# Kernel tuning notes

Hardware: AMD Instinct MI355X
Metric: run time of the kernel (lower is better)

Reference implementation:

```python
import jax, jax.numpy as jnp
import numpy as np

BS, IMG, P, GRID, NPATCH = 4, 224, 14, 16, 256
D, HID, NC, NDIST = 384, 2688, 1000, 7
BETA = 0.07
LN_EPS = 1e-6


def setup_inputs() -> dict:
    key = jax.random.key(0)
    ks = jax.random.split(key, 10)
    feat_target = jax.random.normal(ks[0], (BS, NPATCH, D), jnp.float32)
    feat_ref = jax.random.normal(ks[1], (BS, NPATCH, D), jnp.float32)
    labels_ref = jax.random.randint(ks[2], (BS, 1, IMG, IMG), 0, NC, jnp.int32)
    # distractor permutations of the batch (one per distractor sample)
    perms = jnp.argsort(jax.random.uniform(ks[3], (NDIST, BS)), axis=-1).astype(jnp.int32)
    # projector Mlp (fc1 -> GELU -> fc2), xavier-ish scaling
    fc1_w = jax.random.normal(ks[4], (D, HID), jnp.float32) * (1.0 / np.sqrt(D))
    fc1_b = jnp.zeros((HID,), jnp.float32)
    fc2_w = jax.random.normal(ks[5], (HID, D), jnp.float32) * (1.0 / np.sqrt(HID))
    fc2_b = jnp.zeros((D,), jnp.float32)
    ln_w = jnp.ones((D,), jnp.float32)
    ln_b = jnp.zeros((D,), jnp.float32)
    return {"feat_target": feat_target, "feat_ref": feat_ref, "labels_ref": labels_ref,
            "perms": perms, "fc1_w": fc1_w, "fc1_b": fc1_b, "fc2_w": fc2_w,
            "fc2_b": fc2_b, "ln_w": ln_w, "ln_b": ln_b}


def _layer_norm(x, w, b):
    mu = x.mean(-1, keepdims=True)
    var = jnp.mean((x - mu) ** 2, axis=-1, keepdims=True)
    return (x - mu) * jax.lax.rsqrt(var + LN_EPS) * w + b


def _l2norm(x, eps=1e-12):
    n = jnp.sqrt(jnp.sum(x * x, axis=-1, keepdims=True))
    return x / jnp.maximum(n, eps)


def reference(feat_target, feat_ref, labels_ref, perms, fc1_w, fc1_b, fc2_w, fc2_b, ln_w, ln_b):
    bs = feat_target.shape[0]

    def proj_norm(x):
        h = jax.nn.gelu(x @ fc1_w + fc1_b, approximate=False)  # torch nn.GELU (erf)
        return _layer_norm(h @ fc2_w + fc2_b, ln_w, ln_b)

    ft = proj_norm(feat_target)   # (bs, 256, 384)
    fr = proj_norm(feat_ref)      # (bs, 256, 384)

    # patchify ground truth: (bs,1,224,224) -> (bs, 256, 14*14)
    g = labels_ref.reshape(bs, 1, GRID, P, GRID, P).transpose(0, 2, 4, 1, 3, 5)
    g = g.reshape(bs, NPATCH, P * P)
    # per-patch class histogram / (P*P) == one_hot(...).mean(dim=3), without huge one-hot
    seg = (jnp.arange(NPATCH, dtype=jnp.int32)[None, :, None] * NC + g).reshape(bs, -1)
    counts = jax.vmap(lambda s: jax.ops.segment_sum(
        jnp.ones(s.shape, jnp.float32), s, num_segments=NPATCH * NC))(seg)
    label = counts.reshape(bs, NPATCH, NC) / float(P * P)  # (bs, 256, 1000)

    # distractors: block 0 is identity, blocks 1..NDIST are batch permutations
    all_perm = jnp.concatenate([jnp.arange(bs, dtype=perms.dtype)[None], perms], 0)  # (8, bs)
    lab_d = label[all_perm].transpose(1, 0, 2, 3).reshape(bs, -1, NC)   # (bs, 2048, 1000)
    feat_d = fr[all_perm].transpose(1, 0, 2, 3).reshape(bs, -1, D)      # (bs, 2048, 384)

    # cosine-similarity softmax cross attention (soft kNN over labels)
    q = _l2norm(ft)
    k = _l2norm(feat_d)
    attn = jax.nn.softmax(jnp.einsum('bqd,bkd->bqk', q, k) / BETA, axis=-1)
    label_hat = jnp.einsum('bqk,bkc->bqc', attn, lab_d)                 # (bs, 256, 1000)

    label_hat = label_hat.reshape(bs, GRID, GRID, NC).transpose(0, 3, 1, 2)
    # nearest upsample 16x16 -> 224x224 (scale 14 exactly)
    out = jnp.repeat(jnp.repeat(label_hat, P, axis=2), P, axis=3)
    return out
```

## Files before the change

kernel.cpp:

```cpp
#include <hip/hip_runtime.h>

#define BSZ 4
#define NPATCH 256
#define DIM 384
#define HID 2688
#define NCLS 1000
#define KTOT 2048
#define IMGSZ 224
#define PCH 14
#define GRD 16

static constexpr float INV_BETA = 1.0f / 0.07f;
static constexpr float LN_EPS_F = 1e-6f;

typedef unsigned short u16;
typedef unsigned int   u32;
typedef __attribute__((ext_vector_type(8))) __bf16 bf16x8;
typedef __attribute__((ext_vector_type(4))) float  f32x4;

#define WAITVM(n) asm volatile("s_waitcnt vmcnt(" #n ")" ::: "memory")

__device__ __forceinline__ u16 f2bf(float f) {
    u32 u = __float_as_uint(f);
    return (u16)((u + 0x7FFFu + ((u >> 16) & 1u)) >> 16);
}
__device__ __forceinline__ float bf2f(u16 h) {
    return __uint_as_float(((u32)h) << 16);
}
__device__ __forceinline__ f32x4 mfma16(bf16x8 a, bf16x8 b, f32x4 c) {
    return __builtin_amdgcn_mfma_f32_16x16x32_bf16(a, b, c, 0, 0, 0);
}
__device__ __forceinline__ void gll16(const u16* g, u16* l) {
    __builtin_amdgcn_global_load_lds(
        (const __attribute__((address_space(1))) void*)g,
        (__attribute__((address_space(3))) void*)l, 16, 0, 0);
}
__device__ __forceinline__ bf16x8 ld8(const u16* p) {
    return *(const bf16x8*)p;
}
__device__ __forceinline__ int swz(int row, int cseg) {
    return cseg ^ ((row >> 1) & 3);
}

__device__ __forceinline__ void transpose_split_body(
    const float* __restrict__ In, int R, int C, int bx, int by,
    u16* __restrict__ OutHi, u16* __restrict__ OutLo, float (*tile)[33])
{
    int cx = bx * 32, ry = by * 32;
    int tr = threadIdx.x >> 5, tc = threadIdx.x & 31;
    #pragma unroll
    for (int i = 0; i < 4; ++i)
        tile[tr + i * 8][tc] = In[(size_t)(ry + tr + i * 8) * C + cx + tc];
    __syncthreads();
    #pragma unroll
    for (int i = 0; i < 4; ++i) {
        int orow = cx + tr + i * 8;
        int ocol = ry + tc;
        float v = tile[tc][tr + i * 8];
        u16 h = f2bf(v);
        OutHi[(size_t)orow * R + ocol] = h;
        OutLo[(size_t)orow * R + ocol] = f2bf(v - bf2f(h));
    }
}

__global__ __launch_bounds__(256) void prep_kernel(
    const float* __restrict__ Xt, const float* __restrict__ Xr,
    const float* __restrict__ fc1w, const float* __restrict__ fc2w,
    const int* __restrict__ labels,
    u16* __restrict__ Xhi, u16* __restrict__ Xlo,
    u16* __restrict__ W1Th, u16* __restrict__ W1Tl,
    u16* __restrict__ W2Th, u16* __restrict__ W2Tl,
    u16* __restrict__ LabT)
{
    __shared__ float tile[32][33];
    __shared__ int hist16[16][NCLS];
    int blk = blockIdx.x, t = threadIdx.x;
    if (blk < 768) {
        int e = (blk * 256 + t) * 4;
        const float* src = (e < 1024 * DIM) ? (Xt + e) : (Xr + e - 1024 * DIM);
        float4 v = *(const float4*)src;
        float x[4] = {v.x, v.y, v.z, v.w};
        u16 h[4], l[4];
        #pragma unroll
        for (int i = 0; i < 4; ++i) {
            h[i] = f2bf(x[i]);
            l[i] = f2bf(x[i] - bf2f(h[i]));
        }
        *(uint2*)(Xhi + e) = make_uint2((u32)h[0] | ((u32)h[1] << 16), (u32)h[2] | ((u32)h[3] << 16));
        *(uint2*)(Xlo + e) = make_uint2((u32)l[0] | ((u32)l[1] << 16), (u32)l[2] | ((u32)l[3] << 16));
    } else if (blk < 1776) {
        int i = blk - 768;
        transpose_split_body(fc1w, DIM, HID, i % (HID / 32), i / (HID / 32), W1Th, W1Tl, tile);
    } else if (blk < 2784) {
        int i = blk - 1776;
        transpose_split_body(fc2w, HID, DIM, i % (DIM / 32), i / (DIM / 32), W2Th, W2Tl, tile);
    } else {
        int bp = blk - 2784;
        int b = bp >> 4, py = bp & 15;
        for (int u = t; u < 16 * NCLS; u += 256) ((int*)hist16)[u] = 0;
        __syncthreads();
        const int* lrow = labels + (size_t)b * IMGSZ * IMGSZ + py * PCH * IMGSZ;
        for (int i = t; i < PCH * IMGSZ; i += 256) {
            int lab = lrow[i];
            int px = (i % IMGSZ) / PCH;
            atomicAdd(&hist16[px][lab], 1);
        }
        __syncthreads();
        const float inv = 1.0f / (PCH * PCH);
        for (int u = t; u < 16 * NCLS; u += 256) {
            int c = u >> 4, px = u & 15;
            LabT[((size_t)(b << 10) + c) * 256 + py * 16 + px] =
                f2bf(hist16[px][c] * inv);
        }
    }
}

template<int MODE>
__global__ __launch_bounds__(256) void gemm64(
    const u16* __restrict__ Ahi, const u16* __restrict__ Alo,
    const u16* __restrict__ Bhi, const u16* __restrict__ Blo,
    const float* __restrict__ bias, const int* __restrict__ perms,
    u16* __restrict__ OutHi, u16* __restrict__ OutLo, float* __restrict__ OutF)
{
    constexpr int K  = (MODE == 1) ? HID : DIM;
    constexpr int KS = (MODE == 1) ? HID / 4 : K;
    constexpr int NT = KS / 32;
    constexpr int N  = (MODE == 0) ? HID : (MODE == 1 ? DIM : KTOT);

    __shared__ u16 As_h[3][128 * 32];
    __shared__ u16 As_l[3][128 * 32];
    __shared__ u16 Bs_h[3][64 * 32];
    __shared__ u16 Bs_l[3][64 * 32];

    const int tid = threadIdx.x, lane = tid & 63, wid = tid >> 6;
    const int wm = wid >> 1, wn = wid & 1;
    int n0, m0;
    if constexpr (MODE == 0) {
        int s = (blockIdx.x & 7) * 84 + (blockIdx.x >> 3);
        n0 = (s % 42) * 64;
        m0 = (s / 42) * 128;
    } else {
        n0 = blockIdx.x * 64;
        m0 = blockIdx.y * 128;
    }

    const u16 *a_h, *a_l, *b_h, *b_l;
    if constexpr (MODE == 0) {
        a_h = Ahi + (size_t)m0 * K;   a_l = Alo + (size_t)m0 * K;
        b_h = Bhi + (size_t)n0 * K;   b_l = Blo + (size_t)n0 * K;
    } else if constexpr (MODE == 1) {
        const int kbase = blockIdx.z * KS;
        a_h = Ahi + (size_t)m0 * K + kbase;   a_l = Alo + (size_t)m0 * K + kbase;
        b_h = Bhi + (size_t)n0 * K + kbase;   b_l = Blo + (size_t)n0 * K + kbase;
    } else {
        const int b = blockIdx.z;
        const int d = n0 >> 8;
        const int apd = (d == 0) ? b : perms[(d - 1) * BSZ + b];
        a_h = Ahi + (size_t)(b * NPATCH + m0) * K;
        a_l = Alo + (size_t)(b * NPATCH + m0) * K;
        b_h = Bhi + (size_t)(1024 + apd * NPATCH + (n0 & 255)) * K;
        b_l = Blo + (size_t)(1024 + apd * NPATCH + (n0 & 255)) * K;
    }

    auto stage = [&](int buf, int k0) {
        #pragma unroll
        for (int j = 0; j < 2; ++j) {
            int g = j * 256 + tid;
            int row = g >> 2, cs = g & 3;
            int col = swz(row, cs) << 3;
            gll16(a_h + (size_t)row * K + k0 + col, &As_h[buf][g * 8]);
            gll16(a_l + (size_t)row * K + k0 + col, &As_l[buf][g * 8]);
        }
        {
            int row = tid >> 2, cs = tid & 3;
            int col = swz(row, cs) << 3;
            gll16(b_h + (size_t)row * K + k0 + col, &Bs_h[buf][tid * 8]);
            gll16(b_l + (size_t)row * K + k0 + col, &Bs_l[buf][tid * 8]);
        }
    };

    const int l15 = lane & 15, cq = lane >> 4;
    int aoff[4], boff[2];
    #pragma unroll
    for (int i = 0; i < 4; ++i) {
        int ra = wm * 64 + i * 16 + l15;
        aoff[i] = ra * 32 + swz(ra, cq) * 8;
    }
    #pragma unroll
    for (int j = 0; j < 2; ++j) {
        int rb = wn * 32 + j * 16 + l15;
        boff[j] = rb * 32 + swz(rb, cq) * 8;
    }

    f32x4 acc[4][2] = {};

    auto compute = [&](int buf) {
        bf16x8 ah[4], al[4], bh[2], bl[2];
        #pragma unroll
        for (int i = 0; i < 4; ++i) {
            ah[i] = ld8(&As_h[buf][aoff[i]]);
            al[i] = ld8(&As_l[buf][aoff[i]]);
        }
        #pragma unroll
        for (int j = 0; j < 2; ++j) {
            bh[j] = ld8(&Bs_h[buf][boff[j]]);
            bl[j] = ld8(&Bs_l[buf][boff[j]]);
        }
        #pragma unroll
        for (int mi = 0; mi < 4; ++mi)
            #pragma unroll
            for (int ni = 0; ni < 2; ++ni) {
                acc[mi][ni] = mfma16(ah[mi], bh[ni], acc[mi][ni]);
                acc[mi][ni] = mfma16(ah[mi], bl[ni], acc[mi][ni]);
                acc[mi][ni] = mfma16(al[mi], bh[ni], acc[mi][ni]);
            }
    };

    stage(0, 0);
    stage(1, 32);
    int cur = 0;
    for (int t = 0; t < NT - 1; ++t) {
        WAITVM(6);
        __builtin_amdgcn_s_barrier();
        __builtin_amdgcn_sched_barrier(0);
        if (t + 2 < NT) {
            int nb = cur + 2; if (nb >= 3) nb -= 3;
            stage(nb, (t + 2) * 32);
        }
        compute(cur);
        cur = (cur == 2) ? 0 : cur + 1;
    }
    WAITVM(0);
    __builtin_amdgcn_s_barrier();
    __builtin_amdgcn_sched_barrier(0);
    compute(cur);

    #pragma unroll
    for (int mi = 0; mi < 4; ++mi)
        #pragma unroll
        for (int ni = 0; ni < 2; ++ni)
            #pragma unroll
            for (int r = 0; r < 4; ++r) {
                int gm = m0 + wm * 64 + mi * 16 + cq * 4 + r;
                int gn = n0 + wn * 32 + ni * 16 + l15;
                float v = acc[mi][ni][r];
                if constexpr (MODE == 0) {
                    v += bias[gn];
                    v = 0.5f * v * (1.0f + erff(v * 0.7071067811865476f));
                    u16 h = f2bf(v);
                    OutHi[(size_t)gm * N + gn] = h;
                    OutLo[(size_t)gm * N + gn] = f2bf(v - bf2f(h));
                } else if constexpr (MODE == 1) {
                    OutF[(size_t)blockIdx.z * (2048 * DIM) + (size_t)gm * N + gn] = v;
                } else {
                    float e = expf((v - 1.0f) * INV_BETA);
                    OutHi[((size_t)blockIdx.z * NPATCH + gm) * KTOT + gn] = f2bf(e);
                }
            }
}

__global__ __launch_bounds__(512) void pv_pipe(
    const u16* __restrict__ E, const u16* __restrict__ LabT,
    const int* __restrict__ perms, const float* __restrict__ R,
    float* __restrict__ Lhat)
{
    constexpr int NT = KTOT / 32;
    __shared__ u16 As[3][64 * 32];
    __shared__ u16 Bs[3][64 * 32];
    __shared__ int ap[8];

    const int tid = threadIdx.x, lane = tid & 63, wid = tid >> 6;
    const int wm = wid >> 2, wn = wid & 3;
    const int n0 = blockIdx.x * 64, m0 = blockIdx.y * 64, b = blockIdx.z;
    if (tid < 8) ap[tid] = (tid == 0) ? b : perms[(tid - 1) * BSZ + b];
    __syncthreads();

    const u16* abase = E + (size_t)(b * NPATCH + m0) * KTOT;
    const int cr = (tid & 255) >> 2, ccs = (tid & 255) & 3;
    const int cc = swz(cr, ccs) * 8;

    auto stage = [&](int buf, int k0) {
        if (tid < 256) {
            gll16(abase + (size_t)cr * KTOT + k0 + cc, &As[buf][(tid & 255) * 8]);
        } else {
            int apd = ap[k0 >> 8];
            gll16(LabT + ((size_t)(apd << 10) + n0 + cr) * 256 + (k0 & 255) + cc,
                  &Bs[buf][(tid & 255) * 8]);
        }
    };

    const int l15 = lane & 15, cq = lane >> 4;
    int aoff[2], boff;
    #pragma unroll
    for (int mi = 0; mi < 2; ++mi) {
        int row = wm * 32 + l15 + mi * 16;
        aoff[mi] = row * 32 + swz(row, cq) * 8;
    }
    {
        int row = wn * 16 + l15;
        boff = row * 32 + swz(row, cq) * 8;
    }

    f32x4 acc[2] = {};
    auto compute = [&](int buf) {
        bf16x8 bfr = ld8(&Bs[buf][boff]);
        #pragma unroll
        for (int mi = 0; mi < 2; ++mi) {
            bf16x8 afr = ld8(&As[buf][aoff[mi]]);
            acc[mi] = mfma16(afr, bfr, acc[mi]);
        }
    };

    stage(0, 0);
    stage(1, 32);
    int cur = 0;
    for (int t = 0; t < NT - 1; ++t) {
        WAITVM(1);
        __builtin_amdgcn_s_barrier();
        __builtin_amdgcn_sched_barrier(0);
        if (t + 2 < NT) {
            int nb = cur + 2; if (nb >= 3) nb -= 3;
            stage(nb, (t + 2) * 32);
        }
        compute(cur);
        cur = (cur == 2) ? 0 : cur + 1;
    }
    WAITVM(0);
    __builtin_amdgcn_s_barrier();
    __builtin_amdgcn_sched_barrier(0);
    compute(cur);

    const int gn = n0 + wn * 16 + l15;
    if (gn < NCLS) {
        #pragma unroll
        for (int mi = 0; mi < 2; ++mi)
            #pragma unroll
            for (int r = 0; r < 4; ++r) {
                int gm = m0 + wm * 32 + mi * 16 + ((lane >> 4) << 2) + r;
                float denom = R[(size_t)b * NPATCH + gm];
                Lhat[((size_t)b * NPATCH + gm) * NCLS + gn] = acc[mi][r] / denom;
            }
    }
}

__device__ __forceinline__ float wave_sum(float v) {
    #pragma unroll
    for (int off = 32; off > 0; off >>= 1) v += __shfl_xor(v, off);
    return v;
}

__global__ __launch_bounds__(256) void rowsum_kernel(
    const u16* __restrict__ E, float* __restrict__ R)
{
    int row = blockIdx.x, t = threadIdx.x;
    uint4 u = *(const uint4*)(E + (size_t)row * KTOT + t * 8);
    float s = bf2f(u.x & 0xffff) + bf2f(u.x >> 16)
            + bf2f(u.y & 0xffff) + bf2f(u.y >> 16)
            + bf2f(u.z & 0xffff) + bf2f(u.z >> 16)
            + bf2f(u.w & 0xffff) + bf2f(u.w >> 16);
    s = wave_sum(s);
    __shared__ float red[4];
    if ((t & 63) == 0) red[t >> 6] = s;
    __syncthreads();
    if (t == 0) R[row] = red[0] + red[1] + red[2] + red[3];
}

__global__ __launch_bounds__(256) void ln_l2_kernel(
    const float* __restrict__ P0, const float* __restrict__ fc2b,
    const float* __restrict__ w, const float* __restrict__ b,
    u16* __restrict__ Zhi, u16* __restrict__ Zlo)
{
    const float* P1 = P0 + 1 * 2048 * DIM;
    const float* P2 = P0 + 2 * 2048 * DIM;
    const float* P3 = P0 + 3 * 2048 * DIM;
    int wid = threadIdx.x >> 6, lane = threadIdx.x & 63;
    int row = blockIdx.x * 4 + wid;
    size_t base = (size_t)row * DIM;
    float x[6];
    float s = 0.0f;
    #pragma unroll
    for (int i = 0; i < 6; ++i) {
        int c = lane + 64 * i;
        x[i] = ((P0[base + c] + P1[base + c]) + (P2[base + c] + P3[base + c])) + fc2b[c];
        s += x[i];
    }
    s = wave_sum(s);
    float mu = s * (1.0f / DIM);
    float vs = 0.0f;
    #pragma unroll
    for (int i = 0; i < 6; ++i) { float d = x[i] - mu; vs += d * d; }
    vs = wave_sum(vs);
    float rstd = 1.0f / sqrtf(vs * (1.0f / DIM) + LN_EPS_F);
    float z[6];
    float n2 = 0.0f;
    #pragma unroll
    for (int i = 0; i < 6; ++i) {
        z[i] = (x[i] - mu) * rstd * w[lane + 64 * i] + b[lane + 64 * i];
        n2 += z[i] * z[i];
    }
    n2 = wave_sum(n2);
    float inv = 1.0f / fmaxf(sqrtf(n2), 1e-12f);
    #pragma unroll
    for (int i = 0; i < 6; ++i) {
        float zn = z[i] * inv;
        u16 h = f2bf(zn);
        Zhi[base + lane + 64 * i] = h;
        Zlo[base + lane + 64 * i] = f2bf(zn - bf2f(h));
    }
}

__global__ __launch_bounds__(256) void upsample_kernel(
    const float* __restrict__ Lhat, float* __restrict__ out)
{
    int blk = blockIdx.x;
    int gy = blk & 15;
    int bc = blk >> 4;
    int c = bc % NCLS;
    int b = bc / NCLS;
    __shared__ float vals[GRD];
    int t = threadIdx.x;
    if (t < GRD)
        vals[t] = Lhat[((size_t)(b * NPATCH + gy * GRD + t)) * NCLS + c];
    __syncthreads();
    float* obase = out + ((size_t)(b * NCLS + c) * IMGSZ + gy * PCH) * IMGSZ;
    for (int idx = t; idx < PCH * 56; idx += 256) {
        int x4 = idx % 56, dy = idx / 56;
        int x0 = x4 * 4;
        f32x4 v = {vals[x0 / PCH], vals[(x0 + 1) / PCH],
                   vals[(x0 + 2) / PCH], vals[(x0 + 3) / PCH]};
        __builtin_nontemporal_store(v, (f32x4*)(obase + dy * IMGSZ + x0));
    }
}

extern "C" void kernel_launch(void* const* d_in, const int* in_sizes, int n_in,
                              void* d_out, int out_size, void* d_ws, size_t ws_size,
                              hipStream_t stream)
{
    (void)in_sizes; (void)n_in; (void)out_size; (void)ws_size;
    const float* feat_t = (const float*)d_in[0];
    const float* feat_r = (const float*)d_in[1];
    const int*   labels = (const int*)d_in[2];
    const int*   perms  = (const int*)d_in[3];
    const float* fc1_w  = (const float*)d_in[4];
    const float* fc1_b  = (const float*)d_in[5];
    const float* fc2_w  = (const float*)d_in[6];
    const float* fc2_b  = (const float*)d_in[7];
    const float* ln_w   = (const float*)d_in[8];
    const float* ln_b   = (const float*)d_in[9];
    float* out = (float*)d_out;
    char*  W   = (char*)d_ws;

    u16*   Hhi  = (u16*)(W + 0);
    u16*   Hlo  = (u16*)(W + 11010048);
    u16*   E    = (u16*)(W + 0);
    float* R    = (float*)(W + 4194304);
    float* Lhat = (float*)(W + 4718592);
    float* P0   = (float*)(W + 22020096);
    u16*   Zhi  = (u16*)(W + 34603008);
    u16*   Zlo  = (u16*)(W + 36175872);
    u16*   LabT = (u16*)(W + 37748736);
    u16*   Xhi  = (u16*)(W + 39845888);
    u16*   Xlo  = (u16*)(W + 41418752);
    u16*   W1Th = (u16*)(W + 42991616);
    u16*   W1Tl = (u16*)(W + 45056000);
    u16*   W2Th = (u16*)(W + 47120384);
    u16*   W2Tl = (u16*)(W + 49184768);

    prep_kernel<<<dim3(2848), dim3(256), 0, stream>>>(
        feat_t, feat_r, fc1_w, fc2_w, labels,
        Xhi, Xlo, W1Th, W1Tl, W2Th, W2Tl, LabT);

    gemm64<0><<<dim3(672), dim3(256), 0, stream>>>(
        Xhi, Xlo, W1Th, W1Tl, fc1_b, nullptr, Hhi, Hlo, nullptr);

    gemm64<1><<<dim3(6, 16, 4), dim3(256), 0, stream>>>(
        Hhi, Hlo, W2Th, W2Tl, nullptr, nullptr, nullptr, nullptr, P0);

    ln_l2_kernel<<<dim3(2048 / 4), dim3(256), 0, stream>>>(P0, fc2_b, ln_w, ln_b, Zhi, Zlo);

    gemm64<2><<<dim3(32, 2, 4), dim3(256), 0, stream>>>(
        Zhi, Zlo, Zhi, Zlo, nullptr, perms, E, nullptr, nullptr);

    rowsum_kernel<<<dim3(BSZ * NPATCH), dim3(256), 0, stream>>>(E, R);

    pv_pipe<<<dim3(16, 4, 4), dim3(512), 0, stream>>>(E, LabT, perms, R, Lhat);

    upsample_kernel<<<dim3(BSZ * NCLS * GRD), dim3(256), 0, stream>>>(Lhat, out);
}
```

Measured before the change: 268.4 us.

## Split PV GEMM over K, dedicate QK kernel with 64x64 tiles, vectorize transpose stores

Result: no change. 263.8 us (-1.7%).

```diff
diff --git a/kernel.cpp b/kernel.cpp
--- a/kernel.cpp
+++ b/kernel.cpp
@@ -47,20 +47,25 @@
     u16* __restrict__ OutHi, u16* __restrict__ OutLo, float (*tile)[33])
 {
     int cx = bx * 32, ry = by * 32;
-    int tr = threadIdx.x >> 5, tc = threadIdx.x & 31;
+    int t = threadIdx.x;
+    int tr = t >> 5, tc = t & 31;
     #pragma unroll
     for (int i = 0; i < 4; ++i)
         tile[tr + i * 8][tc] = In[(size_t)(ry + tr + i * 8) * C + cx + tc];
     __syncthreads();
+    int a = t >> 3, seg = t & 7;
+    u16 h4[4], l4[4];
     #pragma unroll
     for (int i = 0; i < 4; ++i) {
-        int orow = cx + tr + i * 8;
-        int ocol = ry + tc;
-        float v = tile[tc][tr + i * 8];
-        u16 h = f2bf(v);
-        OutHi[(size_t)orow * R + ocol] = h;
-        OutLo[(size_t)orow * R + ocol] = f2bf(v - bf2f(h));
-    }
+        float v = tile[seg * 4 + i][a];
+        h4[i] = f2bf(v);
+        l4[i] = f2bf(v - bf2f(h4[i]));
+    }
+    size_t off = (size_t)(cx + a) * R + ry + seg * 4;
+    *(uint2*)(OutHi + off) = make_uint2((u32)h4[0] | ((u32)h4[1] << 16),
+                                        (u32)h4[2] | ((u32)h4[3] << 16));
+    *(uint2*)(OutLo + off) = make_uint2((u32)l4[0] | ((u32)l4[1] << 16),
+                                        (u32)l4[2] | ((u32)l4[3] << 16));
 }
 
 __global__ __launch_bounds__(256) void prep_kernel(
@@ -119,13 +124,13 @@
 __global__ __launch_bounds__(256) void gemm64(
     const u16* __restrict__ Ahi, const u16* __restrict__ Alo,
     const u16* __restrict__ Bhi, const u16* __restrict__ Blo,
-    const float* __restrict__ bias, const int* __restrict__ perms,
+    const float* __restrict__ bias,
     u16* __restrict__ OutHi, u16* __restrict__ OutLo, float* __restrict__ OutF)
 {
     constexpr int K  = (MODE == 1) ? HID : DIM;
     constexpr int KS = (MODE == 1) ? HID / 4 : K;
     constexpr int NT = KS / 32;
-    constexpr int N  = (MODE == 0) ? HID : (MODE == 1 ? DIM : KTOT);
+    constexpr int N  = (MODE == 0) ? HID : DIM;
 
     __shared__ u16 As_h[3][128 * 32];
     __shared__ u16 As_l[3][128 * 32];
@@ -148,18 +153,10 @@
     if constexpr (MODE == 0) {
         a_h = Ahi + (size_t)m0 * K;   a_l = Alo + (size_t)m0 * K;
         b_h = Bhi + (size_t)n0 * K;   b_l = Blo + (size_t)n0 * K;
-    } else if constexpr (MODE == 1) {
+    } else {
         const int kbase = blockIdx.z * KS;
         a_h = Ahi + (size_t)m0 * K + kbase;   a_l = Alo + (size_t)m0 * K + kbase;
         b_h = Bhi + (size_t)n0 * K + kbase;   b_l = Blo + (size_t)n0 * K + kbase;
-    } else {
-        const int b = blockIdx.z;
-        const int d = n0 >> 8;
-        const int apd = (d == 0) ? b : perms[(d - 1) * BSZ + b];
-        a_h = Ahi + (size_t)(b * NPATCH + m0) * K;
-        a_l = Alo + (size_t)(b * NPATCH + m0) * K;
-        b_h = Bhi + (size_t)(1024 + apd * NPATCH + (n0 & 255)) * K;
-        b_l = Blo + (size_t)(1024 + apd * NPATCH + (n0 & 255)) * K;
     }
 
     auto stage = [&](int buf, int k0) {
@@ -250,72 +247,77 @@
                     u16 h = f2bf(v);
                     OutHi[(size_t)gm * N + gn] = h;
                     OutLo[(size_t)gm * N + gn] = f2bf(v - bf2f(h));
-                } else if constexpr (MODE == 1) {
+                } else {
                     OutF[(size_t)blockIdx.z * (2048 * DIM) + (size_t)gm * N + gn] = v;
-                } else {
-                    float e = expf((v - 1.0f) * INV_BETA);
-                    OutHi[((size_t)blockIdx.z * NPATCH + gm) * KTOT + gn] = f2bf(e);
                 }
             }
 }
 
-__global__ __launch_bounds__(512) void pv_pipe(
-    const u16* __restrict__ E, const u16* __restrict__ LabT,
-    const int* __restrict__ perms, const float* __restrict__ R,
-    float* __restrict__ Lhat)
-{
-    constexpr int NT = KTOT / 32;
-    __shared__ u16 As[3][64 * 32];
-    __shared__ u16 Bs[3][64 * 32];
-    __shared__ int ap[8];
+__global__ __launch_bounds__(256) void qk64(
+    const u16* __restrict__ Zhi, const u16* __restrict__ Zlo,
+    const int* __restrict__ perms, u16* __restrict__ E)
+{
+    constexpr int NT = DIM / 32;
+    __shared__ u16 As_h[3][64 * 32];
+    __shared__ u16 As_l[3][64 * 32];
+    __shared__ u16 Bs_h[3][64 * 32];
+    __shared__ u16 Bs_l[3][64 * 32];
 
     const int tid = threadIdx.x, lane = tid & 63, wid = tid >> 6;
-    const int wm = wid >> 2, wn = wid & 3;
+    const int wm = wid >> 1, wn = wid & 1;
     const int n0 = blockIdx.x * 64, m0 = blockIdx.y * 64, b = blockIdx.z;
-    if (tid < 8) ap[tid] = (tid == 0) ? b : perms[(tid - 1) * BSZ + b];
-    __syncthreads();
-
-    const u16* abase = E + (size_t)(b * NPATCH + m0) * KTOT;
-    const int cr = (tid & 255) >> 2, ccs = (tid & 255) & 3;
-    const int cc = swz(cr, ccs) * 8;
+    const int d = n0 >> 8;
+    const int apd = (d == 0) ? b : perms[(d - 1) * BSZ + b];
+
+    const u16* a_h = Zhi + (size_t)(b * NPATCH + m0) * DIM;
+    const u16* a_l = Zlo + (size_t)(b * NPATCH + m0) * DIM;
+    const u16* b_h = Zhi + (size_t)(1024 + apd * NPATCH + (n0 & 255)) * DIM;
+    const u16* b_l = Zlo + (size_t)(1024 + apd * NPATCH + (n0 & 255)) * DIM;
 
     auto stage = [&](int buf, int k0) {
-        if (tid < 256) {
-            gll16(abase + (size_t)cr * KTOT + k0 + cc, &As[buf][(tid & 255) * 8]);
-        } else {
-            int apd = ap[k0 >> 8];
-            gll16(LabT + ((size_t)(apd << 10) + n0 + cr) * 256 + (k0 & 255) + cc,
-                  &Bs[buf][(tid & 255) * 8]);
-        }
+        int row = tid >> 2, cs = tid & 3;
+        int col = swz(row, cs) << 3;
+        gll16(a_h + (size_t)row * DIM + k0 + col, &As_h[buf][tid * 8]);
+        gll16(a_l + (size_t)row * DIM + k0 + col, &As_l[buf][tid * 8]);
+        gll16(b_h + (size_t)row * DIM + k0 + col, &Bs_h[buf][tid * 8]);
+        gll16(b_l + (size_t)row * DIM + k0 + col, &Bs_l[buf][tid * 8]);
     };
 
     const int l15 = lane & 15, cq = lane >> 4;
-    int aoff[2], boff;
-    #pragma unroll
-    for (int mi = 0; mi < 2; ++mi) {
-        int row = wm * 32 + l15 + mi * 16;
-        aoff[mi] = row * 32 + swz(row, cq) * 8;
-    }
-    {
-        int row = wn * 16 + l15;
-        boff = row * 32 + swz(row, cq) * 8;
-    }
-
-    f32x4 acc[2] = {};
+    int aoff[2], boff[2];
+    #pragma unroll
+    for (int i = 0; i < 2; ++i) {
+        int ra = wm * 32 + i * 16 + l15;
+        aoff[i] = ra * 32 + swz(ra, cq) * 8;
+        int rb = wn * 32 + i * 16 + l15;
+        boff[i] = rb * 32 + swz(rb, cq) * 8;
+    }
+
+    f32x4 acc[2][2] = {};
     auto compute = [&](int buf) {
-        bf16x8 bfr = ld8(&Bs[buf][boff]);
-        #pragma unroll
-        for (int mi = 0; mi < 2; ++mi) {
-            bf16x8 afr = ld8(&As[buf][aoff[mi]]);
-            acc[mi] = mfma16(afr, bfr, acc[mi]);
-        }
+        bf16x8 ah[2], al[2], bh[2], bl[2];
+        #pragma unroll
+        for (int i = 0; i < 2; ++i) {
+            ah[i] = ld8(&As_h[buf][aoff[i]]);
+            al[i] = ld8(&As_l[buf][aoff[i]]);
+            bh[i] = ld8(&Bs_h[buf][boff[i]]);
+            bl[i] = ld8(&Bs_l[buf][boff[i]]);
+        }
+        #pragma unroll
+        for (int mi = 0; mi < 2; ++mi)
+            #pragma unroll
+            for (int ni = 0; ni < 2; ++ni) {
+                acc[mi][ni] = mfma16(ah[mi], bh[ni], acc[mi][ni]);
+                acc[mi][ni] = mfma16(ah[mi], bl[ni], acc[mi][ni]);
+                acc[mi][ni] = mfma16(al[mi], bh[ni], acc[mi][ni]);
+            }
     };
 
     stage(0, 0);
     stage(1, 32);
     int cur = 0;
     for (int t = 0; t < NT - 1; ++t) {
-        WAITVM(1);
+        WAITVM(4);
         __builtin_amdgcn_s_barrier();
         __builtin_amdgcn_sched_barrier(0);
         if (t + 2 < NT) {
@@ -330,17 +332,116 @@
     __builtin_amdgcn_sched_barrier(0);
     compute(cur);
 
-    const int gn = n0 + wn * 16 + l15;
-    if (gn < NCLS) {
-        #pragma unroll
-        for (int mi = 0; mi < 2; ++mi)
+    #pragma unroll
+    for (int mi = 0; mi < 2; ++mi)
+        #pragma unroll
+        for (int ni = 0; ni < 2; ++ni)
             #pragma unroll
             for (int r = 0; r < 4; ++r) {
-                int gm = m0 + wm * 32 + mi * 16 + ((lane >> 4) << 2) + r;
-                float denom = R[(size_t)b * NPATCH + gm];
-                Lhat[((size_t)b * NPATCH + gm) * NCLS + gn] = acc[mi][r] / denom;
+                int gm = m0 + wm * 32 + mi * 16 + cq * 4 + r;
+                int gn = n0 + wn * 32 + ni * 16 + l15;
+                float e = expf((acc[mi][ni][r] - 1.0f) * INV_BETA);
+                E[((size_t)b * NPATCH + gm) * KTOT + gn] = f2bf(e);
             }
-    }
+}
+
+__global__ __launch_bounds__(256) void pv64(
+    const u16* __restrict__ E, const u16* __restrict__ LabT,
+    const int* __restrict__ perms, float* __restrict__ Lp)
+{
+    constexpr int KSP = KTOT / 4;
+    constexpr int NT  = KSP / 32;
+    __shared__ u16 As[3][128 * 32];
+    __shared__ u16 Bs[3][64 * 32];
+
+    const int tid = threadIdx.x, lane = tid & 63, wid = tid >> 6;
+    const int wm = wid >> 1, wn = wid & 1;
+    const int n0 = blockIdx.x * 64, m0 = blockIdx.y * 128;
+    const int b = blockIdx.z & 3, ks = blockIdx.z >> 2;
+    const int s0 = ks * 2;
+    const int apd0 = (s0 == 0) ? b : perms[(s0 - 1) * BSZ + b];
+    const int apd1 = perms[s0 * BSZ + b];
+
+    const u16* abase = E + (size_t)(b * NPATCH + m0) * KTOT + ks * KSP;
+
+    auto stage = [&](int buf, int k0) {
+        #pragma unroll
+        for (int j = 0; j < 2; ++j) {
+            int g = j * 256 + tid;
+            int row = g >> 2, cs = g & 3;
+            int col = swz(row, cs) << 3;
+            gll16(abase + (size_t)row * KTOT + k0 + col, &As[buf][g * 8]);
+        }
+        {
+            int apd = (k0 & 256) ? apd1 : apd0;
+            int p0 = k0 & 255;
+            int row = tid >> 2, cs = tid & 3;
+            int col = swz(row, cs) << 3;
+            gll16(LabT + ((size_t)(apd << 10) + n0 + row) * 256 + p0 + col,
+                  &Bs[buf][tid * 8]);
+        }
+    };
+
+    const int l15 = lane & 15, cq = lane >> 4;
+    int aoff[4], boff[2];
+    #pragma unroll
+    for (int i = 0; i < 4; ++i) {
+        int ra = wm * 64 + i * 16 + l15;
+        aoff[i] = ra * 32 + swz(ra, cq) * 8;
+    }
+    #pragma unroll
+    for (int j = 0; j < 2; ++j) {
+        int rb = wn * 32 + j * 16 + l15;
+        boff[j] = rb * 32 + swz(rb, cq) * 8;
+    }
+
+    f32x4 acc[4][2] = {};
+    auto compute = [&](int buf) {
+        bf16x8 a[4], bb[2];
+        #pragma unroll
+        for (int i = 0; i < 4; ++i) a[i] = ld8(&As[buf][aoff[i]]);
+        #pragma unroll
+        for (int j = 0; j < 2; ++j) bb[j] = ld8(&Bs[buf][boff[j]]);
+        #pragma unroll
+        for (int mi = 0; mi < 4; ++mi)
+            #pragma unroll
+            for (int ni = 0; ni < 2; ++ni)
+                acc[mi][ni] = mfma16(a[mi], bb[ni], acc[mi][ni]);
+    };
+
+    stage(0, 0);
+    stage(1, 32);
+    int cur = 0;
+    for (int t = 0; t < NT - 1; ++t) {
+        WAITVM(3);
+        __builtin_amdgcn_s_barrier();
+        __builtin_amdgcn_sched_barrier(0);
+        if (t + 2 < NT) {
+            int nb = cur + 2; if (nb >= 3) nb -= 3;
+            stage(nb, (t + 2) * 32);
+        }
+        compute(cur);
+        cur = (cur == 2) ? 0 : cur + 1;
+    }
+    WAITVM(0);
+    __builtin_amdgcn_s_barrier();
+    __builtin_amdgcn_sched_barrier(0);
+    compute(cur);
+
+    #pragma unroll
+    for (int mi = 0; mi < 4; ++mi)
+        #pragma unroll
+        for (int ni = 0; ni < 2; ++ni) {
+            int gn = n0 + wn * 32 + ni * 16 + l15;
+            if (gn < NCLS) {
+                #pragma unroll
+                for (int r = 0; r < 4; ++r) {
+                    int gm = m0 + wm * 64 + mi * 16 + cq * 4 + r;
+                    Lp[(((size_t)ks * BSZ + b) * NPATCH + gm) * NCLS + gn] =
+                        acc[mi][ni][r];
+                }
+            }
+        }
 }
 
 __device__ __forceinline__ float wave_sum(float v) {
@@ -410,8 +511,10 @@
 }
 
 __global__ __launch_bounds__(256) void upsample_kernel(
-    const float* __restrict__ Lhat, float* __restrict__ out)
-{
+    const float* __restrict__ Lp, const float* __restrict__ R,
+    float* __restrict__ out)
+{
+    constexpr size_t S = (size_t)BSZ * NPATCH * NCLS;
     int blk = blockIdx.x;
     int gy = blk & 15;
     int bc = blk >> 4;
@@ -419,8 +522,11 @@
     int b = bc / NCLS;
     __shared__ float vals[GRD];
     int t = threadIdx.x;
-    if (t < GRD)
-        vals[t] = Lhat[((size_t)(b * NPATCH + gy * GRD + t)) * NCLS + c];
+    if (t < GRD) {
+        int q = b * NPATCH + gy * GRD + t;
+        size_t i = (size_t)q * NCLS + c;
+        vals[t] = ((Lp[i] + Lp[i + S]) + (Lp[i + 2 * S] + Lp[i + 3 * S])) / R[q];
+    }
     __syncthreads();
     float* obase = out + ((size_t)(b * NCLS + c) * IMGSZ + gy * PCH) * IMGSZ;
     for (int idx = t; idx < PCH * 56; idx += 256) {
@@ -454,7 +560,7 @@
     u16*   Hlo  = (u16*)(W + 11010048);
     u16*   E    = (u16*)(W + 0);
     float* R    = (float*)(W + 4194304);
-    float* Lhat = (float*)(W + 4718592);
+    float* Lp   = (float*)(W + 4718592);
     float* P0   = (float*)(W + 22020096);
     u16*   Zhi  = (u16*)(W + 34603008);
     u16*   Zlo  = (u16*)(W + 36175872);
@@ -471,19 +577,18 @@
         Xhi, Xlo, W1Th, W1Tl, W2Th, W2Tl, LabT);
 
     gemm64<0><<<dim3(672), dim3(256), 0, stream>>>(
-        Xhi, Xlo, W1Th, W1Tl, fc1_b, nullptr, Hhi, Hlo, nullptr);
+        Xhi, Xlo, W1Th, W1Tl, fc1_b, Hhi, Hlo, nullptr);
 
     gemm64<1><<<dim3(6, 16, 4), dim3(256), 0, stream>>>(
-        Hhi, Hlo, W2Th, W2Tl, nullptr, nullptr, nullptr, nullptr, P0);
+        Hhi, Hlo, W2Th, W2Tl, nullptr, nullptr, nullptr, P0);
 
     ln_l2_kernel<<<dim3(2048 / 4), dim3(256), 0, stream>>>(P0, fc2_b, ln_w, ln_b, Zhi, Zlo);
 
-    gemm64<2><<<dim3(32, 2, 4), dim3(256), 0, stream>>>(
-        Zhi, Zlo, Zhi, Zlo, nullptr, perms, E, nullptr, nullptr);
+    qk64<<<dim3(32, 4, 4), dim3(256), 0, stream>>>(Zhi, Zlo, perms, E);
 
     rowsum_kernel<<<dim3(BSZ * NPATCH), dim3(256), 0, stream>>>(E, R);
 
-    pv_pipe<<<dim3(16, 4, 4), dim3(512), 0, stream>>>(E, LabT, perms, R, Lhat);
-
-    upsample_kernel<<<dim3(BSZ * NCLS * GRD), dim3(256), 0, stream>>>(Lhat, out);
-}
+    pv64<<<dim3(16, 2, 16), dim3(256), 0, stream>>>(E, LabT, perms, Lp);
+
+    upsample_kernel<<<dim3(BSZ * NCLS * GRD), dim3(256), 0, stream>>>(Lp, R, out);
+}
```
